# Kernel tuning notes

Measured on AMD Instinct MI355X. Metric: run time of the kernel, lower is better.

The kernel has to match this reference:

```python
import jax, jax.numpy as jnp
import numpy as np

BS, NV, D, DFF, E, H = 32, 512, 128, 512, 8, 8
EPS = 1e-5

def layernorm(x, g, b):
    m = x.mean(-1, keepdims=True)
    v = ((x - m) ** 2).mean(-1, keepdims=True)
    return (x - m) / jnp.sqrt(v + EPS) * g + b

def setup_inputs() -> dict:
    key = jax.random.key(0)
    ks = jax.random.split(key, 10)
    s = lambda k, shape: (jax.random.normal(k, shape, jnp.float32) * 0.02)
    return {
        "x": jax.random.normal(ks[0], (BS, NV, D), jnp.float32),
        "cls_emd": jax.random.normal(ks[1], (E, D), jnp.float32),
        "Wq": s(ks[2], (D, D)), "Wk": s(ks[3], (D, D)),
        "Wv": s(ks[4], (D, D)), "Wo": s(ks[5], (D, D)),
        "Wg": s(ks[6], (D, D)),
        "W1": s(ks[7], (E, DFF, 2 * D)), "b1": jnp.zeros((E, DFF), jnp.float32),
        "W2": s(ks[8], (E, D, DFF)), "b2": jnp.zeros((E, D), jnp.float32),
        "g1": jnp.ones((D,), jnp.float32), "be1": jnp.zeros((D,), jnp.float32),
        "g2": jnp.ones((D,), jnp.float32), "be2": jnp.zeros((D,), jnp.float32),
    }

def reference(x, cls_emd, Wq, Wk, Wv, Wo, Wg, W1, b1, W2, b2, g1, be1, g2, be2):
    bs, n, d = x.shape
    dh = d // H
    # --- full multi-head self-attention over the variate axis ---
    q = (x @ Wq).reshape(bs, n, H, dh)
    k = (x @ Wk).reshape(bs, n, H, dh)
    v = (x @ Wv).reshape(bs, n, H, dh)
    scores = jnp.einsum('bnhd,bmhd->bhnm', q, k) * (1.0 / np.sqrt(dh))
    attn = jax.nn.softmax(scores, axis=-1)            # [bs, H, n, n]
    new_x = jnp.einsum('bhnm,bmhd->bnhd', attn, v).reshape(bs, n, d) @ Wo
    # residual + norm1 (dropout = identity in eval)
    x = layernorm(x + new_x, g1, be1)
    # --- gating: per-variate scores over clusters [n_vars, n_clusters] ---
    gate_scores = jax.nn.softmax((x.mean(0) @ Wg) @ cls_emd.T, axis=-1)
    # --- MoE: expand tokens vs every cluster, concat, per-cluster expert MLP ---
    ncl = cls_emd.shape[0]
    y = jnp.broadcast_to(x[:, :, None, :], (bs, n, ncl, d))
    z = jnp.broadcast_to(cls_emd[None, None, :, :], (bs, n, ncl, d))
    yz_cat = jnp.concatenate([y, z], axis=-1)          # [bs, n, K, 2d]
    h = jax.nn.relu(jnp.einsum('bnkc,kfc->bnkf', yz_cat, W1) + b1)  # kernel_size=1 conv == matmul
    expert_out = jnp.einsum('bnkf,kdf->bnkd', h, W2) + b2           # [bs, n, K, d]
    y_r = jnp.einsum('nk,bnkd->bnd', gate_scores, expert_out)
    out = layernorm(x + y_r, g2, be2)
    return (out, attn, gate_scores)
```

## Files before the change

### kernel.cpp

```cpp
#include <hip/hip_runtime.h>
#include <hip/hip_bf16.h>
#include <math.h>

#define BS   32
#define NV   512
#define D    128
#define DFF  512
#define E    8
#define NH   8
#define DH   16
#define M_TOK (BS*NV)
#define EPS  1e-5f

typedef __hip_bfloat16 bf16;
typedef _Float16 f16;
using sh8   = __attribute__((ext_vector_type(8))) short;
using us4   = __attribute__((ext_vector_type(4))) unsigned short;
using h4    = __attribute__((ext_vector_type(4))) _Float16;
using h8    = __attribute__((ext_vector_type(8))) _Float16;
using f32x4 = __attribute__((ext_vector_type(4))) float;
using f32x16 = __attribute__((ext_vector_type(16))) float;

__device__ __forceinline__ float b2f(bf16 v){ return __bfloat162float(v); }
__device__ __forceinline__ bf16  f2b(float v){ return __float2bfloat16(v); }
__device__ __forceinline__ unsigned short f2bu(float v){
    bf16 b = __float2bfloat16(v);
    return __builtin_bit_cast(unsigned short, b);
}

__device__ __forceinline__ void gload_lds16(const void* g, void* l){
    __builtin_amdgcn_global_load_lds(
        (const __attribute__((address_space(1))) unsigned int*)g,
        (__attribute__((address_space(3))) unsigned int*)l, 16, 0, 0);
}

#define PR0 4096
#define PR1 (PR0 + 262144)
#define PR2 (PR1 + 131072)
#define PR3 (PR2 + 524288)
#define PR4 (PR3 + 49152)
#define PR5 (PR4 + 16384)
#define PREP_ITEMS PR5
__global__ __launch_bounds__(256) void k_prep(
    const float* __restrict__ W1, const float* __restrict__ W2,
    const float* __restrict__ x,  const float* __restrict__ Wq,
    const float* __restrict__ Wk, const float* __restrict__ Wv,
    const float* __restrict__ Wo, const float* __restrict__ b1,
    const float* __restrict__ cls,
    bf16* __restrict__ W1b, bf16* __restrict__ W2b, f16* __restrict__ xh,
    f16* __restrict__ WTq, f16* __restrict__ WoT, float* __restrict__ b1eff)
{
    int tid = blockIdx.x*256 + threadIdx.x;
    if (tid < PR0){
        int e = tid >> 9, f = tid & 511;
        float acc = b1[e*DFF + f];
        const float* wrow = W1 + ((size_t)e*DFF + f)*(2*D) + D;
        #pragma unroll 8
        for (int c=0;c<D;++c) acc += cls[e*D+c] * wrow[c];
        b1eff[tid] = acc;
    } else if (tid < PR1){
        int i = (tid - PR0)*4;
        float4 vv = *(const float4*)(W1 + i);
        us4 o; o[0]=f2bu(vv.x); o[1]=f2bu(vv.y); o[2]=f2bu(vv.z); o[3]=f2bu(vv.w);
        *(us4*)(W1b + i) = o;
    } else if (tid < PR2){
        int i = (tid - PR1)*4;
        float4 vv = *(const float4*)(W2 + i);
        us4 o; o[0]=f2bu(vv.x); o[1]=f2bu(vv.y); o[2]=f2bu(vv.z); o[3]=f2bu(vv.w);
        *(us4*)(W2b + i) = o;
    } else if (tid < PR3){
        int i = (tid - PR2)*4;
        float4 vv = *(const float4*)(x + i);
        h4 o; o[0]=(f16)vv.x; o[1]=(f16)vv.y; o[2]=(f16)vv.z; o[3]=(f16)vv.w;
        *(h4*)(xh + i) = o;
    } else if (tid < PR4){
        int idx = tid - PR3;
        int c = idx>>7, kk = idx&127;
        int which = c>>7, col = c&127;
        const float* W = which==0?Wq:(which==1?Wk:Wv);
        WTq[idx] = (f16)W[kk*D + col];
    } else if (tid < PR5){
        int idx = tid - PR4;
        int c = idx>>7, kk = idx&127;
        WoT[idx] = (f16)Wo[kk*D + c];
    }
}

__global__ __launch_bounds__(512) void k_qkv_mfma(
    const f16* __restrict__ xh, const f16* __restrict__ WT,
    f16* __restrict__ q, f16* __restrict__ k, f16* __restrict__ v)
{
    __shared__ __align__(16) char smem[65536];
    char* Xl = smem;
    char* Wl = smem + 16384;
    int t = threadIdx.x;
    int w = t>>6, lane = t&63;
    int bm = blockIdx.x, nh = blockIdx.y;

    const f16* xsrc = xh + (size_t)bm*64*D;
    #pragma unroll
    for (int i=0;i<2;++i){
        int ci = i*512 + t;
        int row = ci>>4, c16 = (ci&15)^(row&7);
        gload_lds16(xsrc + row*D + c16*8, Xl + (size_t)(i*512 + w*64)*16);
    }
    const f16* wsrc = WT + (size_t)nh*192*D;
    #pragma unroll
    for (int i=0;i<6;++i){
        int ci = i*512 + t;
        int row = ci>>4, c16 = (ci&15)^(row&7);
        gload_lds16(wsrc + row*D + c16*8, Wl + (size_t)(i*512 + w*64)*16);
    }
    __syncthreads();

    int rblk = w>>1, ch = w&1;
    int rl = lane&15, g = lane>>4;

    h8 afr[4];
    #pragma unroll
    for (int kk=0;kk<4;++kk){
        int row = rblk*16 + rl;
        int bo = (row<<8) + (kk<<6) + (g<<4); bo ^= (row&7)<<4;
        afr[kk] = *(const h8*)(Xl + bo);
    }
    f32x4 acc[6];
    #pragma unroll
    for (int nt=0;nt<6;++nt) acc[nt] = (f32x4){0.f,0.f,0.f,0.f};
    #pragma unroll
    for (int nt=0; nt<6; ++nt){
        #pragma unroll
        for (int kk=0;kk<4;++kk){
            int row = ch*96 + nt*16 + rl;
            int bo = (row<<8)+(kk<<6)+(g<<4); bo ^= (row&7)<<4;
            h8 bfr = *(const h8*)(Wl + bo);
            acc[nt] = __builtin_amdgcn_mfma_f32_16x16x32_f16(afr[kk], bfr, acc[nt],0,0,0);
        }
    }
    #pragma unroll
    for (int nt=0;nt<6;++nt){
        int cidx = nh*192 + ch*96 + nt*16 + rl;
        int which = cidx>>7, hh=(cidx>>4)&7, d = cidx&15;
        f16* dst = which==0?q:(which==1?k:v);
        #pragma unroll
        for (int j=0;j<4;++j){
            int m = bm*64 + rblk*16 + g*4 + j;
            int b = m>>9, n = m&511;
            dst[(((size_t)(b*NH+hh))*NV + n)*DH + d] = (f16)acc[nt][j];
        }
    }
}

#define KSTRIDE 24
#define VSTRIDE 520
#define PSTRIDE 68
__global__ __launch_bounds__(256) void k_attn2(
    const f16* __restrict__ q, const f16* __restrict__ kin, const f16* __restrict__ vin,
    float* __restrict__ attn_out, f16* __restrict__ ctx)
{
    __shared__ f16  Kl[512*KSTRIDE];
    __shared__ f16  VT[16*VSTRIDE];
    __shared__ f16  pbh[4][16*PSTRIDE];

    int bh = blockIdx.x;
    int t  = threadIdx.x;
    const f16* kb = kin + (size_t)bh*NV*DH;
    const f16* vb = vin + (size_t)bh*NV*DH;

    {
        int r0 = t*2;
        #pragma unroll
        for (int rr=0; rr<2; ++rr){
            const uint4* src = (const uint4*)(kb + (size_t)(r0+rr)*DH);
            *((uint4*)(Kl + (r0+rr)*KSTRIDE))     = src[0];
            *((uint4*)(Kl + (r0+rr)*KSTRIDE + 8)) = src[1];
        }
        const unsigned short* v0s = (const unsigned short*)(vb + (size_t)r0*DH);
        const unsigned short* v1s = v0s + DH;
        #pragma unroll
        for (int d=0; d<DH; ++d){
            unsigned u = (unsigned)v0s[d] | ((unsigned)v1s[d] << 16);
            *((unsigned*)(VT + d*VSTRIDE + r0)) = u;
        }
    }
    __syncthreads();

    int wave = t >> 6, lane = t & 63;
    int ql = lane & 15, g = lane >> 4;
    int q0 = blockIdx.y*64 + wave*16;

    h4 qf = *(const h4*)(q + ((size_t)bh*NV + q0 + ql)*DH + 4*g);
    #pragma unroll
    for (int i=0;i<4;++i) qf[i] = qf[i] * (_Float16)0.36067376f;

    f32x4 S[32];
    #pragma unroll
    for (int tt=0; tt<32; ++tt){
        h4 kf = *(const h4*)(Kl + (tt*16 + ql)*KSTRIDE + 4*g);
        S[tt] = __builtin_amdgcn_mfma_f32_16x16x16f16(kf, qf, (f32x4){0.f,0.f,0.f,0.f}, 0,0,0);
    }

    float sum = 0.f;
    #pragma unroll
    for (int tt=0; tt<32; ++tt)
        #pragma unroll
        for (int j=0;j<4;++j){
            float p = exp2f(S[tt][j]);
            S[tt][j] = p; sum += p;
        }
    sum += __shfl_xor(sum, 16);
    sum += __shfl_xor(sum, 32);
    float inv = 1.f/sum;
    #pragma unroll
    for (int tt=0; tt<32; ++tt)
        #pragma unroll
        for (int j=0;j<4;++j) S[tt][j] *= inv;

    f32x4 o0 = (f32x4){0.f,0.f,0.f,0.f}, o1 = (f32x4){0.f,0.f,0.f,0.f};
    f16* pw = pbh[wave];
    float* attnbase = attn_out + ((size_t)bh*NV + q0)*NV;
    int col16 = lane & 15, qg = lane >> 4;
    #pragma unroll
    for (int c=0; c<8; ++c){
        #pragma unroll
        for (int tt2=0; tt2<4; ++tt2){
            int tt = c*4 + tt2;
            h4 pf;
            pf[0]=(f16)S[tt][0]; pf[1]=(f16)S[tt][1];
            pf[2]=(f16)S[tt][2]; pf[3]=(f16)S[tt][3];
            h4 vf = *(const h4*)(VT + ql*VSTRIDE + tt*16 + 4*g);
            if (tt&1) o1 = __builtin_amdgcn_mfma_f32_16x16x16f16(vf, pf, o1, 0,0,0);
            else      o0 = __builtin_amdgcn_mfma_f32_16x16x16f16(vf, pf, o0, 0,0,0);
            *(h4*)(pw + ql*PSTRIDE + tt2*16 + 4*g) = pf;
        }
        asm volatile("" ::: "memory");
        #pragma unroll
        for (int rr=0; rr<4; ++rr){
            int qq = rr*4 + qg;
            h4 hv = *(const h4*)(pw + qq*PSTRIDE + col16*4);
            f32x4 vv;
            vv[0]=(float)hv[0]; vv[1]=(float)hv[1];
            vv[2]=(float)hv[2]; vv[3]=(float)hv[3];
            __builtin_nontemporal_store(vv, (f32x4*)(attnbase + (size_t)qq*NV + c*64 + col16*4));
        }
        asm volatile("" ::: "memory");
    }
    f32x4 o = o0 + o1;
    int b = bh >> 3, h = bh & 7;
    f16* cb = ctx + ((size_t)(b*NV) + q0 + ql)*D + h*DH + 4*g;
    h4 oc; oc[0]=(f16)o[0]; oc[1]=(f16)o[1]; oc[2]=(f16)o[2]; oc[3]=(f16)o[3];
    *(h4*)cb = oc;
}

__global__ __launch_bounds__(512) void k_woln_mfma(
    const f16* __restrict__ ctx, const f16* __restrict__ WoT,
    const float* __restrict__ x, const float* __restrict__ g1, const float* __restrict__ be1,
    bf16* __restrict__ x1b, float* __restrict__ yacc)
{
    __shared__ __align__(16) char smem[49152];
    __shared__ float lnred[2][64][2];
    char* Cl = smem;
    char* Wl = smem + 16384;
    int t = threadIdx.x;
    int w = t>>6, lane = t&63;
    int bm = blockIdx.x;

    const f16* csrc = ctx + (size_t)bm*64*D;
    #pragma unroll
    for (int i=0;i<2;++i){
        int ci = i*512 + t;
        int row = ci>>4, c16 = (ci&15)^(row&7);
        gload_lds16(csrc + row*D + c16*8, Cl + (size_t)(i*512 + w*64)*16);
    }
    #pragma unroll
    for (int i=0;i<4;++i){
        int ci = i*512 + t;
        int row = ci>>4, c16 = (ci&15)^(row&7);
        gload_lds16(WoT + row*D + c16*8, Wl + (size_t)(i*512 + w*64)*16);
    }
    __syncthreads();

    int rblk = w>>1, ch = w&1;
    int rl = lane&15, g = lane>>4;

    h8 afr[4];
    #pragma unroll
    for (int kk=0;kk<4;++kk){
        int row = rblk*16 + rl;
        int bo = (row<<8) + (kk<<6) + (g<<4); bo ^= (row&7)<<4;
        afr[kk] = *(const h8*)(Cl + bo);
    }
    f32x4 acc[4];
    #pragma unroll
    for (int nt=0;nt<4;++nt) acc[nt] = (f32x4){0.f,0.f,0.f,0.f};
    #pragma unroll
    for (int nt=0; nt<4; ++nt){
        #pragma unroll
        for (int kk=0;kk<4;++kk){
            int row = ch*64 + nt*16 + rl;
            int bo = (row<<8)+(kk<<6)+(g<<4); bo ^= (row&7)<<4;
            h8 bfr = *(const h8*)(Wl + bo);
            acc[nt] = __builtin_amdgcn_mfma_f32_16x16x32_f16(afr[kk], bfr, acc[nt],0,0,0);
        }
    }

    float rowv[4][4];
    #pragma unroll
    for (int j=0;j<4;++j){
        int m = bm*64 + rblk*16 + g*4 + j;
        #pragma unroll
        for (int dt=0;dt<4;++dt){
            int d = ch*64 + dt*16 + rl;
            rowv[j][dt] = acc[dt][j] + x[(size_t)m*D + d];
        }
    }
    #pragma unroll
    for (int j=0;j<4;++j){
        float s  = rowv[j][0]+rowv[j][1]+rowv[j][2]+rowv[j][3];
        float s2 = rowv[j][0]*rowv[j][0]+rowv[j][1]*rowv[j][1]
                 + rowv[j][2]*rowv[j][2]+rowv[j][3]*rowv[j][3];
        #pragma unroll
        for (int o=1;o<16;o<<=1){ s += __shfl_xor(s,o); s2 += __shfl_xor(s2,o); }
        if (rl==0){
            int row = rblk*16 + g*4 + j;
            lnred[ch][row][0] = s;
            lnred[ch][row][1] = s2;
        }
    }
    __syncthreads();
    #pragma unroll
    for (int j=0;j<4;++j){
        int row = rblk*16 + g*4 + j;
        float S  = lnred[0][row][0] + lnred[1][row][0];
        float S2 = lnred[0][row][1] + lnred[1][row][1];
        float mean = S*(1.f/D);
        float var  = S2*(1.f/D) - mean*mean;
        float rs = rsqrtf(var + EPS);
        int m = bm*64 + row;
        #pragma unroll
        for (int dt=0;dt<4;++dt){
            int d = ch*64 + dt*16 + rl;
            float o1 = (rowv[j][dt]-mean)*rs*g1[d] + be1[d];
            x1b[(size_t)m*D + d] = f2b(o1);
            yacc[(size_t)m*D + d] = o1;
        }
    }
}

__global__ __launch_bounds__(128) void k_gate(
    const float* __restrict__ yacc, const float* __restrict__ Wg, const float* __restrict__ cls,
    float* __restrict__ gate, float* __restrict__ gate_out)
{
    __shared__ float xm[D];
    __shared__ float tt[D];
    __shared__ float se[E];
    int n = blockIdx.x, t = threadIdx.x;
    float s = 0.f;
    #pragma unroll
    for (int b=0;b<BS;++b) s += yacc[((size_t)b*NV + n)*D + t];
    xm[t] = s * (1.f/BS);
    __syncthreads();
    float a = 0.f;
    for (int c=0;c<D;++c) a += xm[c] * Wg[c*D + t];
    tt[t] = a;
    __syncthreads();
    if (t < E){
        float acc=0.f;
        for (int c=0;c<D;++c) acc += tt[c] * cls[t*D + c];
        se[t]=acc;
    }
    __syncthreads();
    if (t==0){
        float mx=se[0];
        for(int e=1;e<E;++e) mx=fmaxf(mx,se[e]);
        float sm=0.f; float p[E];
        for(int e=0;e<E;++e){ p[e]=__expf(se[e]-mx); sm+=p[e]; }
        float inv=1.f/sm;
        for(int e=0;e<E;++e){
            gate[n*E+e]     = p[e]*inv;
            gate_out[n*E+e] = p[e]*inv;
        }
    }
}

__global__ __launch_bounds__(512) void k_moe_fused(
    const bf16* __restrict__ x1b, const bf16* __restrict__ W1b, const bf16* __restrict__ W2b,
    const float* __restrict__ b1eff, const float* __restrict__ b2,
    const float* __restrict__ gate, const float* __restrict__ yacc,
    const float* __restrict__ g2, const float* __restrict__ be2,
    float* __restrict__ out)
{
    __shared__ __align__(16) char smem[147456];
    char* Hl = smem + 131072;
    float (*lnred)[4][2] = (float (*)[4][2])Hl;

    int t = threadIdx.x;
    int w = t >> 6, lane = t & 63;
    int mb = w >> 2, nb = w & 3;
    int l31 = lane & 31, h = lane >> 5;
    int bm = blockIdx.x;

    sh8 afr[8];
    {
        const bf16* Ab = x1b + (size_t)(bm*64 + mb*32 + l31)*D;
        #pragma unroll
        for (int s=0;s<8;++s) afr[s] = *(const sh8*)(Ab + s*16 + h*8);
    }

    f32x16 oacc = {};
    f32x16 acc2e = {};

    auto STAGE = [&](int idx, int buf){
        int e = idx >> 2, fc = idx & 3;
        const bf16* w1src = W1b + ((size_t)e*DFF + fc*128)*(2*D);
        const bf16* w2src = W2b + (size_t)e*D*DFF + fc*128;
        char* Wa = smem + buf*65536;
        char* Wb = Wa + 32768;
        #pragma unroll
        for (int i=0;i<4;++i){
            int ci  = (i*8 + w)*64 + lane;
            int row = ci >> 4;
            int c16 = (ci & 15) ^ (row & 7);
            gload_lds16(w1src + (size_t)row*256 + c16*8, Wa + (size_t)(i*8+w)*1024);
            gload_lds16(w2src + (size_t)row*512 + c16*8, Wb + (size_t)(i*8+w)*1024);
        }
    };

    STAGE(0, 0);
    asm volatile("s_waitcnt vmcnt(0)" ::: "memory");
    __syncthreads();

    for (int idx=0; idx<32; ++idx){
        int buf = idx & 1;
        int e = idx >> 2, fc = idx & 3;
        char* Wa = smem + buf*65536;
        char* Wb = Wa + 32768;

        if (idx < 31) STAGE(idx+1, buf^1);

        f32x16 acc1 = {};
        {
            int row = nb*32 + l31;
            int rbase = (row<<8);
            int swz = (row&7)<<4;
            #pragma unroll
            for (int s=0;s<8;++s){
                int bo = (rbase + s*32 + h*16) ^ swz;
                sh8 bfr = *(const sh8*)(Wa + bo);
                acc1 = __builtin_amdgcn_mfma_f32_32x32x16_bf16(afr[s], bfr, acc1, 0,0,0);
            }
        }
        {
            float bia = b1eff[e*DFF + fc*128 + nb*32 + l31];
            #pragma unroll
            for (int r=0;r<16;++r){
                int rowm = mb*32 + (r&3) + 8*(r>>2) + 4*h;
                float v = acc1[r] + bia;
                v = v > 0.f ? v : 0.f;
                int bo = (rowm<<8) + ((nb*32 + l31)<<1);
                bo ^= (rowm&7)<<4;
                *(bf16*)(Hl + bo) = f2b(v);
            }
        }
        __syncthreads();

        {
            int rowh = mb*32 + l31;
            int hbase = (rowh<<8), hswz = (rowh&7)<<4;
            int roww = nb*32 + l31;
            int wbase = (roww<<8), wswz = (roww&7)<<4;
            #pragma unroll
            for (int s=0;s<8;++s){
                sh8 hfr = *(const sh8*)(Hl + ((hbase + s*32 + h*16) ^ hswz));
                sh8 wfr = *(const sh8*)(Wb + ((wbase + s*32 + h*16) ^ wswz));
                acc2e = __builtin_amdgcn_mfma_f32_32x32x16_bf16(hfr, wfr, acc2e, 0,0,0);
            }
        }

        if (fc == 3){
            int d = nb*32 + l31;
            float bia2 = b2[e*D + d];
            #pragma unroll
            for (int r=0;r<16;++r){
                int m = bm*64 + mb*32 + (r&3) + 8*(r>>2) + 4*h;
                float gv = gate[(m & 511)*E + e];
                oacc[r] += gv*(acc2e[r] + bia2);
            }
            acc2e = (f32x16){};
        }

        asm volatile("s_waitcnt vmcnt(0)" ::: "memory");
        __syncthreads();
    }

    int d = nb*32 + l31;
    float rowv[16];
    #pragma unroll
    for (int r=0;r<16;++r){
        int m = bm*64 + mb*32 + (r&3) + 8*(r>>2) + 4*h;
        rowv[r] = oacc[r] + yacc[(size_t)m*D + d];
    }
    #pragma unroll
    for (int r=0;r<16;++r){
        float s = rowv[r], s2 = rowv[r]*rowv[r];
        #pragma unroll
        for (int o=1;o<32;o<<=1){ s += __shfl_xor(s,o); s2 += __shfl_xor(s2,o); }
        if (l31==0){
            int rowl = mb*32 + (r&3) + 8*(r>>2) + 4*h;
            lnred[rowl][nb][0] = s;
            lnred[rowl][nb][1] = s2;
        }
    }
    __syncthreads();
    #pragma unroll
    for (int r=0;r<16;++r){
        int rowl = mb*32 + (r&3) + 8*(r>>2) + 4*h;
        float S  = lnred[rowl][0][0]+lnred[rowl][1][0]+lnred[rowl][2][0]+lnred[rowl][3][0];
        float S2 = lnred[rowl][0][1]+lnred[rowl][1][1]+lnred[rowl][2][1]+lnred[rowl][3][1];
        float mean = S*(1.f/D);
        float var  = S2*(1.f/D) - mean*mean;
        float rs = rsqrtf(var + EPS);
        int m = bm*64 + rowl;
        out[(size_t)m*D + d] = (rowv[r]-mean)*rs*g2[d] + be2[d];
    }
}

extern "C" void kernel_launch(void* const* d_in, const int* in_sizes, int n_in,
                              void* d_out, int out_size, void* d_ws, size_t ws_size,
                              hipStream_t stream)
{
    const float* x   = (const float*)d_in[0];
    const float* cls = (const float*)d_in[1];
    const float* Wq  = (const float*)d_in[2];
    const float* Wk  = (const float*)d_in[3];
    const float* Wv  = (const float*)d_in[4];
    const float* Wo  = (const float*)d_in[5];
    const float* Wg  = (const float*)d_in[6];
    const float* W1  = (const float*)d_in[7];
    const float* b1  = (const float*)d_in[8];
    const float* W2  = (const float*)d_in[9];
    const float* b2  = (const float*)d_in[10];
    const float* g1  = (const float*)d_in[11];
    const float* be1 = (const float*)d_in[12];
    const float* g2  = (const float*)d_in[13];
    const float* be2 = (const float*)d_in[14];

    float* out      = (float*)d_out;
    float* attn     = out + (size_t)M_TOK*D;
    float* gate_out = attn + (size_t)BS*NH*NV*NV;

    char* ws = (char*)d_ws;
    size_t off = 0;
    auto alloc = [&](size_t bytes)->void*{ void* p = ws + off; off += (bytes + 255) & ~(size_t)255; return p; };
    f16*   q    = (f16*)  alloc((size_t)M_TOK*D*2);
    f16*   kbuf = (f16*)  alloc((size_t)M_TOK*D*2);
    f16*   vbuf = (f16*)  alloc((size_t)M_TOK*D*2);
    f16*   ctx  = (f16*)  alloc((size_t)M_TOK*D*2);
    bf16*  x1b  = (bf16*) alloc((size_t)M_TOK*D*2);
    float* yacc = (float*)alloc((size_t)M_TOK*D*4);
    float* gate = (float*)alloc((size_t)NV*E*4);
    float* b1eff= (float*)alloc((size_t)E*DFF*4);
    bf16*  W1b  = (bf16*) alloc((size_t)E*DFF*2*D*2);
    bf16*  W2b  = (bf16*) alloc((size_t)E*D*DFF*2);
    f16*   xh   = (f16*)  alloc((size_t)M_TOK*D*2);
    f16*   WTq  = (f16*)  alloc((size_t)384*D*2);
    f16*   WoT  = (f16*)  alloc((size_t)D*D*2);

    k_prep<<<(PREP_ITEMS+255)/256, 256, 0, stream>>>(
        W1, W2, x, Wq, Wk, Wv, Wo, b1, cls,
        W1b, W2b, xh, WTq, WoT, b1eff);

    k_qkv_mfma<<<dim3(M_TOK/64, 2), 512, 0, stream>>>(xh, WTq, q, kbuf, vbuf);
    k_attn2<<<dim3(BS*NH, NV/64), 256, 0, stream>>>(q, kbuf, vbuf, attn, ctx);
    k_woln_mfma<<<M_TOK/64, 512, 0, stream>>>(ctx, WoT, x, g1, be1, x1b, yacc);
    k_gate<<<NV, 128, 0, stream>>>(yacc, Wg, cls, gate, gate_out);
    k_moe_fused<<<256, 512, 0, stream>>>(x1b, W1b, W2b, b1eff, b2, gate, yacc, g2, be2, out);
}
```

Measured before the change: 165.7 us.

## Pack softmax probabilities as fp16 and reuse K LDS for staging to raise occupancy

The attention kernel now computes exp2 right after each QK MFMA and keeps the unnormalized probabilities as packed fp16 instead of 32 fp32 vectors. This roughly halves score register usage, and launch bounds request 4 blocks per CU. The per-wave probability staging buffer now aliases the K shared-memory tile after a barrier, and the K row stride shrinks to 20, which cuts LDS footprint. Normalisation happens in fp16 after rounding, which may add small precision error in the attention output.

```diff
diff --git a/kernel.cpp b/kernel.cpp
--- a/kernel.cpp
+++ b/kernel.cpp
@@ -150,16 +150,15 @@
     }
 }
 
-#define KSTRIDE 24
+#define KSTRIDE 20
 #define VSTRIDE 520
 #define PSTRIDE 68
-__global__ __launch_bounds__(256) void k_attn2(
+__global__ __launch_bounds__(256, 4) void k_attn2(
     const f16* __restrict__ q, const f16* __restrict__ kin, const f16* __restrict__ vin,
     float* __restrict__ attn_out, f16* __restrict__ ctx)
 {
     __shared__ f16  Kl[512*KSTRIDE];
     __shared__ f16  VT[16*VSTRIDE];
-    __shared__ f16  pbh[4][16*PSTRIDE];
 
     int bh = blockIdx.x;
     int t  = threadIdx.x;
@@ -170,9 +169,9 @@
         int r0 = t*2;
         #pragma unroll
         for (int rr=0; rr<2; ++rr){
-            const uint4* src = (const uint4*)(kb + (size_t)(r0+rr)*DH);
-            *((uint4*)(Kl + (r0+rr)*KSTRIDE))     = src[0];
-            *((uint4*)(Kl + (r0+rr)*KSTRIDE + 8)) = src[1];
+            const uint2* src = (const uint2*)(kb + (size_t)(r0+rr)*DH);
+            uint2* dst = (uint2*)(Kl + (r0+rr)*KSTRIDE);
+            dst[0]=src[0]; dst[1]=src[1]; dst[2]=src[2]; dst[3]=src[3];
         }
         const unsigned short* v0s = (const unsigned short*)(vb + (size_t)r0*DH);
         const unsigned short* v1s = v0s + DH;
@@ -192,31 +191,26 @@
     #pragma unroll
     for (int i=0;i<4;++i) qf[i] = qf[i] * (_Float16)0.36067376f;
 
-    f32x4 S[32];
+    h4 P16[32];
+    float sum = 0.f;
     #pragma unroll
     for (int tt=0; tt<32; ++tt){
         h4 kf = *(const h4*)(Kl + (tt*16 + ql)*KSTRIDE + 4*g);
-        S[tt] = __builtin_amdgcn_mfma_f32_16x16x16f16(kf, qf, (f32x4){0.f,0.f,0.f,0.f}, 0,0,0);
-    }
-
-    float sum = 0.f;
-    #pragma unroll
-    for (int tt=0; tt<32; ++tt)
-        #pragma unroll
-        for (int j=0;j<4;++j){
-            float p = exp2f(S[tt][j]);
-            S[tt][j] = p; sum += p;
-        }
+        f32x4 S = __builtin_amdgcn_mfma_f32_16x16x16f16(kf, qf, (f32x4){0.f,0.f,0.f,0.f}, 0,0,0);
+        float p0 = exp2f(S[0]), p1 = exp2f(S[1]), p2 = exp2f(S[2]), p3 = exp2f(S[3]);
+        sum += (p0+p1) + (p2+p3);
+        h4 ph; ph[0]=(f16)p0; ph[1]=(f16)p1; ph[2]=(f16)p2; ph[3]=(f16)p3;
+        P16[tt] = ph;
+    }
     sum += __shfl_xor(sum, 16);
     sum += __shfl_xor(sum, 32);
     float inv = 1.f/sum;
-    #pragma unroll
-    for (int tt=0; tt<32; ++tt)
-        #pragma unroll
-        for (int j=0;j<4;++j) S[tt][j] *= inv;
+    f16 hinv = (f16)inv;
+
+    __syncthreads();
 
     f32x4 o0 = (f32x4){0.f,0.f,0.f,0.f}, o1 = (f32x4){0.f,0.f,0.f,0.f};
-    f16* pw = pbh[wave];
+    f16* pw = ((f16*)Kl) + wave*(16*PSTRIDE);
     float* attnbase = attn_out + ((size_t)bh*NV + q0)*NV;
     int col16 = lane & 15, qg = lane >> 4;
     #pragma unroll
@@ -224,9 +218,9 @@
         #pragma unroll
         for (int tt2=0; tt2<4; ++tt2){
             int tt = c*4 + tt2;
-            h4 pf;
-            pf[0]=(f16)S[tt][0]; pf[1]=(f16)S[tt][1];
-            pf[2]=(f16)S[tt][2]; pf[3]=(f16)S[tt][3];
+            h4 pf = P16[tt];
+            pf[0] = pf[0]*hinv; pf[1] = pf[1]*hinv;
+            pf[2] = pf[2]*hinv; pf[3] = pf[3]*hinv;
             h4 vf = *(const h4*)(VT + ql*VSTRIDE + tt*16 + 4*g);
             if (tt&1) o1 = __builtin_amdgcn_mfma_f32_16x16x16f16(vf, pf, o1, 0,0,0);
             else      o0 = __builtin_amdgcn_mfma_f32_16x16x16f16(vf, pf, o0, 0,0,0);
```

Measured after the change: 184.2 us. +11.1%, slower.
